# Kernel optimization log

Hardware: AMD Instinct MI355X
Metric: run time of the kernel (lower is better)

Reference implementation:

```python
import jax, jax.numpy as jnp
import numpy as np

N_HEADS = 16
LN_EPS = 1e-5

def layer_norm(x, w):
    # matches torch LayerNorm in fp32, weight-only (no bias)
    x = x.astype(jnp.float32)
    mu = jnp.mean(x, axis=-1, keepdims=True)
    var = jnp.mean((x - mu) ** 2, axis=-1, keepdims=True)
    return (x - mu) / jnp.sqrt(var + LN_EPS) * w

def rotate_half(t):
    t1, t2 = jnp.split(t, 2, axis=-1)
    return jnp.concatenate((-t2, t1), axis=-1)

def setup_inputs() -> dict:
    key = jax.random.key(0)
    ks = jax.random.split(key, 16)
    B, S, D, C = 2, 2048, 1024, 1024
    H = N_HEADS
    hd = D // H
    # rotary tables: emb = cat(freqs, freqs), freqs = t * inv_freq
    inv_freq = 1.0 / (10000.0 ** (np.arange(0, hd, 2, dtype=np.float32) / hd))
    t = np.arange(S, dtype=np.float32)
    freqs = np.outer(t, inv_freq)                       # [S, hd/2]
    emb = np.concatenate([freqs, freqs], axis=-1)       # [S, hd]
    s = 0.02
    return {
        "x": jax.random.normal(ks[0], (B, S, D), jnp.float32),
        "rotary_cos": jnp.asarray(np.cos(emb)),
        "rotary_sin": jnp.asarray(np.sin(emb)),
        "c": jax.random.normal(ks[1], (B, C), jnp.float32),
        "norm1_w": jnp.ones((D,), jnp.float32),
        "qkv_w": jax.random.normal(ks[2], (3 * D, D), jnp.float32) * s,
        "out_w": jax.random.normal(ks[3], (D, D), jnp.float32) * s,
        "norm2_w": jnp.ones((D,), jnp.float32),
        "fc1_w": jax.random.normal(ks[4], (4 * D, D), jnp.float32) * s,
        "fc1_b": jnp.zeros((4 * D,), jnp.float32),
        "fc2_w": jax.random.normal(ks[5], (D, 4 * D), jnp.float32) * s,
        "fc2_b": jnp.zeros((D,), jnp.float32),
        # NOTE: module zero-inits adaLN; random here for a non-degenerate baseline
        "ada_w": jax.random.normal(ks[6], (6 * D, C), jnp.float32) * s,
        "ada_b": jnp.zeros((6 * D,), jnp.float32),
    }

def reference(x, rotary_cos, rotary_sin, c, norm1_w, qkv_w, out_w, norm2_w,
              fc1_w, fc1_b, fc2_w, fc2_b, ada_w, ada_b):
    B, S, D = x.shape
    H = N_HEADS
    hd = D // H
    # AdaLN conditioning -> six [B,1,D] modulation tensors
    mods = (c @ ada_w.T + ada_b)[:, None, :]                       # [B,1,6D]
    shift_msa, scale_msa, gate_msa, shift_mlp, scale_mlp, gate_mlp = jnp.split(mods, 6, axis=2)
    x_skip = x
    # LN + modulate + QKV
    h = layer_norm(x, norm1_w) * (1.0 + scale_msa) + shift_msa     # [B,S,D]
    qkv = (h @ qkv_w.T).reshape(B, S, 3, H, hd)
    # rotary applied to packed qkv (q, k, and v) as in the torchscript fallback
    cos = rotary_cos[None, :, None, None, :]                       # [1,S,1,1,hd]
    sin = rotary_sin[None, :, None, None, :]
    qkv = qkv * cos + rotate_half(qkv) * sin
    q, k, v = qkv[:, :, 0], qkv[:, :, 1], qkv[:, :, 2]             # [B,S,H,hd]
    scale = hd ** -0.5
    scores = jnp.einsum('bqhd,bkhd->bhqk', q, k) * scale           # [B,H,S,S]
    attn = jax.nn.softmax(scores, axis=-1)
    o = jnp.einsum('bhqk,bkhd->bqhd', attn, v).reshape(B, S, D)
    # gated residual (dropout=0 / eval)
    x = gate_msa * (o @ out_w.T) + x_skip
    # second LN + modulate + MLP (exact gelu, matching F.gelu default)
    h2 = layer_norm(x, norm2_w) * (1.0 + scale_mlp) + shift_mlp
    mlp = jax.nn.gelu(h2 @ fc1_w.T + fc1_b, approximate=False) @ fc2_w.T + fc2_b
    return gate_mlp * mlp + x
```

## Files before the change

### kernel.cpp

```cpp
#include <hip/hip_runtime.h>
#include <hip/hip_bf16.h>


typedef unsigned short u16;
typedef unsigned int   u32;
typedef __bf16 bf16x8 __attribute__((ext_vector_type(8)));
typedef float  f32x4  __attribute__((ext_vector_type(4)));

#define MFMA_BF16(a, b, c) __builtin_amdgcn_mfma_f32_16x16x32_bf16((a), (b), (c), 0, 0, 0)

__device__ __forceinline__ float b2f(u16 u) {
    union { u32 i; float f; } v; v.i = ((u32)u) << 16; return v.f;
}
__device__ __forceinline__ u16 f2b(float f) {
    union { u32 i; float f; } v; v.f = f;
    u32 i = v.i;
    return (u16)((i + 0x7FFFu + ((i >> 16) & 1u)) >> 16);
}
__device__ __forceinline__ u32 pk2(float a, float b) {
#if __has_builtin(__builtin_amdgcn_cvt_pk_bf16_f32)
    typedef __bf16 bf16x2_t __attribute__((ext_vector_type(2)));
    union { bf16x2_t v; u32 u; } cv;
    cv.v = __builtin_amdgcn_cvt_pk_bf16_f32(a, b);
    return cv.u;
#else
    return (u32)f2b(a) | ((u32)f2b(b) << 16);
#endif
}
__device__ __forceinline__ float finz(float v) {
    return __builtin_isfinite(v) ? v : 0.0f;
}
__device__ __forceinline__ void dma16(const void* g, void* l) {
    __builtin_amdgcn_global_load_lds(
        (const __attribute__((address_space(1))) unsigned int*)(uintptr_t)g,
        (__attribute__((address_space(3))) unsigned int*)(uintptr_t)l,
        16, 0, 0);
}

__global__ __launch_bounds__(256) void convert_kernel(
    const float* __restrict__ in, u16* __restrict__ out, int n8, int kshift)
{
    int i = blockIdx.x * 256 + threadIdx.x;
    if (i >= n8) return;
    size_t o = (size_t)i * 8;
    int bk   = (int)(o >> (kshift + 7));
    int rem  = (int)(o & (((size_t)128 << kshift) - 1));
    int kg   = rem >> 10;
    int nloc = (rem >> 3) & 127;
    const float* src = in + (((size_t)bk * 128 + nloc) << kshift) + kg * 8;
    float4 a = *(const float4*)src;
    float4 b = *(const float4*)(src + 4);
    union { u16 s[8]; float4 v; } wp;
    wp.s[0] = f2b(a.x); wp.s[1] = f2b(a.y); wp.s[2] = f2b(a.z); wp.s[3] = f2b(a.w);
    wp.s[4] = f2b(b.x); wp.s[5] = f2b(b.y); wp.s[6] = f2b(b.z); wp.s[7] = f2b(b.w);
    *(float4*)(out + o) = wp.v;
}

__global__ __launch_bounds__(64) void mods_kernel(
    const float* __restrict__ c, const float* __restrict__ ada_w,
    const float* __restrict__ ada_b, float* __restrict__ mods)
{
    const int n = blockIdx.x;
    const int lane = threadIdx.x;
    const float* wr = ada_w + (size_t)n * 1024;
    float a0 = 0.f, a1 = 0.f;
    for (int k = lane; k < 1024; k += 64) {
        float w = wr[k];
        a0 += w * c[k];
        a1 += w * c[1024 + k];
    }
    for (int o = 32; o > 0; o >>= 1) {
        a0 += __shfl_down(a0, o, 64);
        a1 += __shfl_down(a1, o, 64);
    }
    if (lane == 0) {
        float bb = ada_b[n];
        mods[n]        = a0 + bb;
        mods[6144 + n] = a1 + bb;
    }
}

__global__ __launch_bounds__(256) void ln_mod_kernel(
    const u16* __restrict__ xbf, const float* __restrict__ xf,
    const float* __restrict__ w, const float* __restrict__ mods,
    int scale_off, int shift_off, u16* __restrict__ out)
{
    const int row = blockIdx.x;
    const int b   = row >> 11;
    const int tid = threadIdx.x;
    const size_t base = (size_t)row * 1024 + tid * 4;
    float v[4];
    if (xf) {
        float4 t = *(const float4*)(xf + base);
        v[0] = t.x; v[1] = t.y; v[2] = t.z; v[3] = t.w;
    } else {
        uint2 p = *(const uint2*)(xbf + base);
        union { u32 i; float f; } a, bb, cc, d;
        a.i  = p.x << 16;          v[0] = a.f;
        bb.i = p.x & 0xFFFF0000u;  v[1] = bb.f;
        cc.i = p.y << 16;          v[2] = cc.f;
        d.i  = p.y & 0xFFFF0000u;  v[3] = d.f;
    }
    float s  = v[0] + v[1] + v[2] + v[3];
    float sq = v[0]*v[0] + v[1]*v[1] + v[2]*v[2] + v[3]*v[3];
    __shared__ float rs[256], rq[256];
    rs[tid] = s; rq[tid] = sq;
    __syncthreads();
    for (int o = 128; o > 0; o >>= 1) {
        if (tid < o) { rs[tid] += rs[tid + o]; rq[tid] += rq[tid + o]; }
        __syncthreads();
    }
    const float mean = rs[0] * (1.0f / 1024.0f);
    const float var  = rq[0] * (1.0f / 1024.0f) - mean * mean;
    const float inv  = rsqrtf(fmaxf(var, 0.f) + 1e-5f);
    union { u16 s4[4]; uint2 u2; } pk;
    for (int i = 0; i < 4; ++i) {
        int cidx = tid * 4 + i;
        float y = (v[i] - mean) * inv * w[cidx];
        y = y * (1.0f + mods[b * 6144 + scale_off + cidx]) + mods[b * 6144 + shift_off + cidx];
        pk.s4[i] = f2b(y);
    }
    size_t o = ((size_t)(row >> 7)) * 131072 + ((tid * 4) >> 3) * 1024
             + (row & 127) * 8 + ((tid * 4) & 7);
    *(uint2*)(out + o) = pk.u2;
}

template<int MODE>
__global__ __launch_bounds__(256) void gemm128(
    const u16* __restrict__ A, const u16* __restrict__ W,
    int M, int N, int K,
    const float* __restrict__ mods, const float* __restrict__ bias,
    const float* __restrict__ resid_f, const u16* __restrict__ resid_bf,
    float* __restrict__ out_f, u16* __restrict__ out_bf,
    u16* __restrict__ aux1, u16* __restrict__ aux2,
    const float* __restrict__ rcos, const float* __restrict__ rsin)
{
    __shared__ u16 As[2][4096];
    __shared__ u16 Bs[2][4096];
    const int tid  = threadIdx.x;
    const int wave = tid >> 6, lane = tid & 63;
    const int quad = lane >> 4, l15 = lane & 15;
    const int wi = wave >> 1, wj = wave & 1;

    const int gx  = gridDim.x;
    const int nwg = gx * gridDim.y;
    const int d   = blockIdx.y * gx + blockIdx.x;
    const int t   = (d & 7) * (nwg >> 3) + (d >> 3);
    const int m0  = (t / gx) * 128, n0 = (t % gx) * 128;

    f32x4 acc[4][4] = {};

    const u16* Asrc = A + (size_t)m0 * K + wave * 1024 + lane * 8;
    const u16* Bsrc = W + (size_t)n0 * K + wave * 1024 + lane * 8;
    const int wo = wave * 1024;

    dma16(Asrc,       &As[0][wo]);
    dma16(Asrc + 512, &As[0][wo + 512]);
    dma16(Bsrc,       &Bs[0][wo]);
    dma16(Bsrc + 512, &Bs[0][wo + 512]);
    __syncthreads();

    const int nt = K >> 5;
    for (int tt = 0; tt < nt; ++tt) {
        const int cur = tt & 1;
        if (tt + 1 < nt) {
            const u16* a = Asrc + (size_t)(tt + 1) * 4096;
            const u16* b = Bsrc + (size_t)(tt + 1) * 4096;
            dma16(a,       &As[cur ^ 1][wo]);
            dma16(a + 512, &As[cur ^ 1][wo + 512]);
            dma16(b,       &Bs[cur ^ 1][wo]);
            dma16(b + 512, &Bs[cur ^ 1][wo + 512]);
        }
        bf16x8 af[4], bw[4];
        #pragma unroll
        for (int f = 0; f < 4; ++f) {
            af[f] = *(const bf16x8*)(&As[cur][quad * 1024 + (wi * 64 + f * 16 + l15) * 8]);
            bw[f] = *(const bf16x8*)(&Bs[cur][quad * 1024 + (wj * 64 + f * 16 + l15) * 8]);
        }
        #pragma unroll
        for (int fi = 0; fi < 4; ++fi)
            #pragma unroll
            for (int fj = 0; fj < 4; ++fj)
                acc[fi][fj] = MFMA_BF16(af[fi], bw[fj], acc[fi][fj]);
        __syncthreads();
    }

    if (MODE == 4) {
        const int colbase = n0 + wj * 64;
        const int wcol = colbase >> 10;
        const int hh   = (colbase & 1023) >> 6;
        #pragma unroll
        for (int fi = 0; fi < 4; ++fi) {
            const int rbase = m0 + wi * 64 + fi * 16 + quad * 4;
            #pragma unroll
            for (int reg = 0; reg < 4; ++reg) {
                const int r = rbase + reg;
                const int b = r >> 11, s = r & 2047;
                const int bh = b * 16 + hh;
                #pragma unroll
                for (int fj = 0; fj < 2; ++fj) {
                    const int d2 = fj * 16 + l15;
                    float va = acc[fi][fj][reg];
                    float vb = acc[fi][fj + 2][reg];
                    float ca = rcos[s * 64 + d2];
                    float sa = rsin[s * 64 + d2];
                    float ra = va * ca - vb * sa;
                    float rb = vb * ca + va * sa;
                    if (wcol == 0) {
                        ra *= 0.125f; rb *= 0.125f;
                        u16* dst = aux1 + ((size_t)bh * 2048 + s) * 64;
                        dst[d2]      = f2b(ra);
                        dst[d2 + 32] = f2b(rb);
                    } else if (wcol == 1) {
                        size_t base = (size_t)bh * 131072 + (s >> 6) * 4096
                                    + (s & 63) * 8 + (d2 & 7);
                        aux2[base + (d2 >> 3) * 512]        = f2b(ra);
                        aux2[base + ((d2 >> 3) + 4) * 512]  = f2b(rb);
                    } else {
                        size_t base = (size_t)bh * 131072 + (s >> 6) * 4096
                                    + ((s & 63) >> 3) * 512 + (s & 7);
                        out_bf[base + d2 * 8]        = f2b(ra);
                        out_bf[base + (d2 + 32) * 8] = f2b(rb);
                    }
                }
            }
        }
        return;
    }

    #pragma unroll
    for (int fi = 0; fi < 4; ++fi) {
        #pragma unroll
        for (int fj = 0; fj < 4; ++fj) {
            const int cidx  = n0 + wj * 64 + fj * 16 + l15;
            const int rbase = m0 + wi * 64 + fi * 16 + quad * 4;
            #pragma unroll
            for (int reg = 0; reg < 4; ++reg) {
                const int r = rbase + reg;
                float v = acc[fi][fj][reg];
                if (MODE == 1) {
                    float u = v + bias[cidx];
                    float g = 0.5f * u * (1.0f + erff(u * 0.70710678118654752f));
                    size_t o = ((size_t)(r >> 7)) * 524288 + (cidx >> 3) * 1024
                             + (r & 127) * 8 + (cidx & 7);
                    out_bf[o] = f2b(g);
                } else if (MODE == 2) {
                    int bb = r >> 11;
                    float gate = mods[bb * 6144 + 2048 + cidx];
                    out_bf[(size_t)r * N + cidx] = f2b(gate * v + resid_f[(size_t)r * N + cidx]);
                } else if (MODE == 3) {
                    int bb = r >> 11;
                    float u = v + bias[cidx];
                    float gate = mods[bb * 6144 + 5120 + cidx];
                    out_f[(size_t)r * N + cidx] =
                        finz(gate * u + b2f(resid_bf[(size_t)r * N + cidx]));
                }
            }
        }
    }
}

__global__ __launch_bounds__(256) void attn_kernel(
    const u16* __restrict__ Q, const u16* __restrict__ Kb,
    const u16* __restrict__ Vb, u16* __restrict__ O)
{
    __shared__ u16 Ks[4096];
    __shared__ u16 Vs[4096];
    __shared__ u16 Ps[4][16 * 72];
    const int tid  = threadIdx.x;
    const int wave = tid >> 6, lane = tid & 63;
    const int quad = lane >> 4, l15 = lane & 15;
    const int bh = blockIdx.x & 31, qt = blockIdx.x >> 5;

    const u16* Qh = Q  + ((size_t)bh * 2048 + qt * 64) * 64;
    const u16* Kh = Kb + (size_t)bh * 131072;
    const u16* Vh = Vb + (size_t)bh * 131072;

    bf16x8 aq[2];
    #pragma unroll
    for (int kh = 0; kh < 2; ++kh)
        aq[kh] = *(const bf16x8*)(Qh + (size_t)(wave * 16 + l15) * 64 + kh * 32 + quad * 8);

    f32x4 acc_o[4] = {};
    float lsum[4] = {0.f, 0.f, 0.f, 0.f};

    for (int kb = 0; kb < 32; ++kb) {
        __syncthreads();
        const u16* kc = Kh + kb * 4096;
        const u16* vc = Vh + kb * 4096;
        dma16(kc + (2 * wave) * 512 + lane * 8,     &Ks[(2 * wave) * 512]);
        dma16(kc + (2 * wave + 1) * 512 + lane * 8, &Ks[(2 * wave + 1) * 512]);
        dma16(vc + (2 * wave) * 512 + lane * 8,     &Vs[(2 * wave) * 512]);
        dma16(vc + (2 * wave + 1) * 512 + lane * 8, &Vs[(2 * wave + 1) * 512]);
        __syncthreads();

        f32x4 sc[4] = {};
        #pragma unroll
        for (int kt = 0; kt < 4; ++kt)
            #pragma unroll
            for (int kh = 0; kh < 2; ++kh) {
                bf16x8 bk = *(const bf16x8*)(&Ks[(quad + kh * 4) * 512 + (kt * 16 + l15) * 8]);
                sc[kt] = MFMA_BF16(aq[kh], bk, sc[kt]);
            }

        #pragma unroll
        for (int kt = 0; kt < 4; ++kt)
            #pragma unroll
            for (int reg = 0; reg < 4; ++reg)
                sc[kt][reg] = __expf(fminf(sc[kt][reg], 50.f));
        #pragma unroll
        for (int reg = 0; reg < 4; ++reg)
            lsum[reg] += (sc[0][reg] + sc[1][reg]) + (sc[2][reg] + sc[3][reg]);

        #pragma unroll
        for (int kt = 0; kt < 4; kt += 2)
            #pragma unroll
            for (int reg = 0; reg < 4; ++reg) {
                u32 p = pk2(sc[kt][reg], sc[kt + 1][reg]);
                Ps[wave][(quad * 4 + reg) * 72 + kt * 16 + l15]       = (u16)p;
                Ps[wave][(quad * 4 + reg) * 72 + (kt + 1) * 16 + l15] = (u16)(p >> 16);
            }
        __asm volatile("s_waitcnt lgkmcnt(0)" ::: "memory");

        bf16x8 ap0 = *(const bf16x8*)(&Ps[wave][l15 * 72 + quad * 8]);
        bf16x8 ap1 = *(const bf16x8*)(&Ps[wave][l15 * 72 + 32 + quad * 8]);
        #pragma unroll
        for (int dt = 0; dt < 4; ++dt) {
            bf16x8 bv0 = *(const bf16x8*)(&Vs[quad * 512 + (dt * 16 + l15) * 8]);
            bf16x8 bv1 = *(const bf16x8*)(&Vs[(quad + 4) * 512 + (dt * 16 + l15) * 8]);
            acc_o[dt] = MFMA_BF16(ap0, bv0, acc_o[dt]);
            acc_o[dt] = MFMA_BF16(ap1, bv1, acc_o[dt]);
        }
    }

    float linv[4];
    #pragma unroll
    for (int reg = 0; reg < 4; ++reg) {
        float l = lsum[reg];
        l += __shfl_xor(l, 1, 64);
        l += __shfl_xor(l, 2, 64);
        l += __shfl_xor(l, 4, 64);
        l += __shfl_xor(l, 8, 64);
        linv[reg] = 1.0f / l;
    }

    const int b = bh >> 4, hh = bh & 15;
    #pragma unroll
    for (int dt = 0; dt < 4; ++dt)
        #pragma unroll
        for (int reg = 0; reg < 4; ++reg) {
            int q = qt * 64 + wave * 16 + quad * 4 + reg;
            int r = b * 2048 + q;
            int col = hh * 64 + dt * 16 + l15;
            float v = acc_o[dt][reg] * linv[reg];
            O[((size_t)(r >> 7)) * 131072 + (col >> 3) * 1024
              + (r & 127) * 8 + (col & 7)] = f2b(v);
        }
}

extern "C" void kernel_launch(void* const* d_in, const int* in_sizes, int n_in,
                              void* d_out, int out_size, void* d_ws, size_t ws_size,
                              hipStream_t stream)
{
    const float* x     = (const float*)d_in[0];
    const float* rcos  = (const float*)d_in[1];
    const float* rsin  = (const float*)d_in[2];
    const float* c     = (const float*)d_in[3];
    const float* n1w   = (const float*)d_in[4];
    const float* qkvw  = (const float*)d_in[5];
    const float* outw  = (const float*)d_in[6];
    const float* n2w   = (const float*)d_in[7];
    const float* fc1w  = (const float*)d_in[8];
    const float* fc1b  = (const float*)d_in[9];
    const float* fc2w  = (const float*)d_in[10];
    const float* fc2b  = (const float*)d_in[11];
    const float* adaw  = (const float*)d_in[12];
    const float* adab  = (const float*)d_in[13];
    float* out = (float*)d_out;

    char* ws = (char*)d_ws;
    const size_t MB8 = (size_t)8 * 1024 * 1024;
    float* mods  = (float*)ws;
    u16*   W     = (u16*)(ws + 49152);
    char*  S1    = ws + 49152 + MB8;
    char*  S2    = S1 + MB8;

    u16* h    = (u16*)d_out;
    u16* qs   = (u16*)S1;
    u16* ks   = (u16*)S2;
    u16* vT   = (u16*)(S2 + MB8);
    u16* ob   = (u16*)d_out;
    u16* x2   = (u16*)S1;
    u16* h2   = (u16*)d_out;
    u16* mid  = (u16*)S2;

    mods_kernel<<<6144, 64, 0, stream>>>(c, adaw, adab, mods);
    ln_mod_kernel<<<4096, 256, 0, stream>>>(nullptr, x, n1w, mods, 1024, 0, h);
    convert_kernel<<<1536, 256, 0, stream>>>(qkvw, W, 393216, 10);
    gemm128<4><<<dim3(24, 32), 256, 0, stream>>>(h, W, 4096, 3072, 1024,
        nullptr, nullptr, nullptr, nullptr, nullptr, vT, qs, ks, rcos, rsin);
    attn_kernel<<<1024, 256, 0, stream>>>(qs, ks, vT, ob);
    convert_kernel<<<512, 256, 0, stream>>>(outw, W, 131072, 10);
    gemm128<2><<<dim3(8, 32), 256, 0, stream>>>(ob, W, 4096, 1024, 1024,
        mods, nullptr, x, nullptr, nullptr, x2, nullptr, nullptr, nullptr, nullptr);
    ln_mod_kernel<<<4096, 256, 0, stream>>>(x2, nullptr, n2w, mods, 4096, 3072, h2);
    convert_kernel<<<2048, 256, 0, stream>>>(fc1w, W, 524288, 10);
    gemm128<1><<<dim3(32, 32), 256, 0, stream>>>(h2, W, 4096, 4096, 1024,
        nullptr, fc1b, nullptr, nullptr, nullptr, mid, nullptr, nullptr, nullptr, nullptr);
    convert_kernel<<<2048, 256, 0, stream>>>(fc2w, W, 524288, 12);
    gemm128<3><<<dim3(8, 32), 256, 0, stream>>>(mid, W, 4096, 1024, 4096,
        mods, fc2b, nullptr, x2, out, nullptr, nullptr, nullptr, nullptr, nullptr);
}
```

Measured before the change: 445.0 us.

## Triple-buffer GEMM LDS tiles with vmcnt waits and drop tile swizzle

Moves the GEMM K-loop from double to triple buffering in LDS, so async global-to-LDS loads are issued two tiles ahead. It uses explicit s_waitcnt vmcnt counts plus a single barrier per iteration in place of a trailing __syncthreads. It also replaces the XCD-aware blockIdx remapping with a plain row/column mapping. The aim is to hide more memory latency and cut one barrier per iteration, at the cost of extra LDS (lower occupancy) and possibly worse L2 locality across chiplets.

New measurement: 421.8 us. 1.05x faster.

```diff
diff --git a/kernel.cpp b/kernel.cpp
--- a/kernel.cpp
+++ b/kernel.cpp
@@ -135,18 +135,13 @@
     u16* __restrict__ aux1, u16* __restrict__ aux2,
     const float* __restrict__ rcos, const float* __restrict__ rsin)
 {
-    __shared__ u16 As[2][4096];
-    __shared__ u16 Bs[2][4096];
+    __shared__ u16 As[3][4096];
+    __shared__ u16 Bs[3][4096];
     const int tid  = threadIdx.x;
     const int wave = tid >> 6, lane = tid & 63;
     const int quad = lane >> 4, l15 = lane & 15;
     const int wi = wave >> 1, wj = wave & 1;
-
-    const int gx  = gridDim.x;
-    const int nwg = gx * gridDim.y;
-    const int d   = blockIdx.y * gx + blockIdx.x;
-    const int t   = (d & 7) * (nwg >> 3) + (d >> 3);
-    const int m0  = (t / gx) * 128, n0 = (t % gx) * 128;
+    const int m0 = blockIdx.y * 128, n0 = blockIdx.x * 128;
 
     f32x4 acc[4][4] = {};
 
@@ -154,22 +149,30 @@
     const u16* Bsrc = W + (size_t)n0 * K + wave * 1024 + lane * 8;
     const int wo = wave * 1024;
 
-    dma16(Asrc,       &As[0][wo]);
-    dma16(Asrc + 512, &As[0][wo + 512]);
-    dma16(Bsrc,       &Bs[0][wo]);
-    dma16(Bsrc + 512, &Bs[0][wo + 512]);
-    __syncthreads();
+    auto stage = [&](int tt, int buf) {
+        const u16* a = Asrc + (size_t)tt * 4096;
+        const u16* b = Bsrc + (size_t)tt * 4096;
+        dma16(a,       &As[buf][wo]);
+        dma16(a + 512, &As[buf][wo + 512]);
+        dma16(b,       &Bs[buf][wo]);
+        dma16(b + 512, &Bs[buf][wo + 512]);
+    };
 
     const int nt = K >> 5;
-    for (int tt = 0; tt < nt; ++tt) {
-        const int cur = tt & 1;
-        if (tt + 1 < nt) {
-            const u16* a = Asrc + (size_t)(tt + 1) * 4096;
-            const u16* b = Bsrc + (size_t)(tt + 1) * 4096;
-            dma16(a,       &As[cur ^ 1][wo]);
-            dma16(a + 512, &As[cur ^ 1][wo + 512]);
-            dma16(b,       &Bs[cur ^ 1][wo]);
-            dma16(b + 512, &Bs[cur ^ 1][wo + 512]);
+    stage(0, 0);
+    stage(1, 1);
+
+    int cur = 0;
+    for (int t = 0; t < nt; ++t) {
+        if (t + 1 < nt) {
+            __asm volatile("s_waitcnt vmcnt(4)" ::: "memory");
+        } else {
+            __asm volatile("s_waitcnt vmcnt(0)" ::: "memory");
+        }
+        __builtin_amdgcn_s_barrier();
+        if (t + 2 < nt) {
+            int nb = cur + 2; if (nb >= 3) nb -= 3;
+            stage(t + 2, nb);
         }
         bf16x8 af[4], bw[4];
         #pragma unroll
@@ -182,7 +185,7 @@
             #pragma unroll
             for (int fj = 0; fj < 4; ++fj)
                 acc[fi][fj] = MFMA_BF16(af[fi], bw[fj], acc[fi][fj]);
-        __syncthreads();
+        cur = (cur + 1 == 3) ? 0 : cur + 1;
     }
 
     if (MODE == 4) {
```
